# Kernel optimization log

Hardware: AMD Instinct MI355X
Metric: run time of the kernel (lower is better)

## Reference

```python
import jax, jax.numpy as jnp
import numpy as np

# ---- static config (mirrors GptOssDecoderLayer init) ----
H = 1024      # hidden_size
HD = 64       # head_size
NQ = 16       # num_query_heads
NKV = 4       # num_key_value_heads
G = NQ // NKV # num_key_value_groups
E = 8         # num_experts
TOPK = 2      # experts_per_token
FFN = 1024    # expert intermediate (== hidden in GPT-OSS)
B, Q = 4, 128 # batch sequences, new query tokens per sequence
P, PS = 8, 128
S = P * PS    # kv length per sequence
T = B * Q     # total query tokens
SW = 128      # sliding window (layer_idx % 2 == 0 -> active)
LIMIT = 7.0   # swiglu_limit
ALPHA = 1.702
EPS = 1e-5
NEG = -1e30
SCALE = HD ** -0.5


def rmsnorm(x, w):
    return x * w * jax.lax.rsqrt(jnp.mean(x * x, axis=-1, keepdims=True) + EPS)


def setup_inputs() -> dict:
    key = jax.random.key(0)
    ks = jax.random.split(key, 16)
    hidden = jax.random.normal(ks[0], (T, H), jnp.float32)
    kv_cache = jax.random.normal(ks[1], (B * P, 2, PS, NKV, HD), jnp.float32)
    kv_page_indices = jnp.arange(B * P, dtype=jnp.int32).reshape(B, P)
    # additive causal mask: query q sits at absolute position S - Q + q
    qpos = S - Q + jnp.arange(Q)
    kpos = jnp.arange(S)
    causal = qpos[:, None] >= kpos[None, :]
    attention_mask = jnp.broadcast_to(
        jnp.where(causal, 0.0, NEG).astype(jnp.float32), (B, Q, S))
    sinks = 0.1 * jax.random.normal(ks[2], (NQ,), jnp.float32)
    w_qkv = jax.random.normal(ks[3], (H, HD * (NQ + 2 * NKV)), jnp.float32) / np.sqrt(H)
    b_qkv = jnp.zeros((HD * (NQ + 2 * NKV),), jnp.float32)
    w_o = jax.random.normal(ks[4], (NQ * HD, H), jnp.float32) / np.sqrt(NQ * HD)
    b_o = jnp.zeros((H,), jnp.float32)
    ln1_w = jnp.ones((H,), jnp.float32)
    ln2_w = jnp.ones((H,), jnp.float32)
    w_router = jax.random.normal(ks[5], (H, E), jnp.float32) / np.sqrt(H)
    b_router = jnp.zeros((E,), jnp.float32)
    w_gate_up = jax.random.normal(ks[6], (E, H, 2 * FFN), jnp.float32) / np.sqrt(H)
    b_gate_up = jnp.zeros((E, 2 * FFN), jnp.float32)
    w_down = jax.random.normal(ks[7], (E, FFN, H), jnp.float32) / np.sqrt(FFN)
    b_down = jnp.zeros((E, H), jnp.float32)
    return dict(hidden=hidden, kv_cache=kv_cache, attention_mask=attention_mask,
                kv_page_indices=kv_page_indices, sinks=sinks, w_qkv=w_qkv,
                b_qkv=b_qkv, w_o=w_o, b_o=b_o, ln1_w=ln1_w, ln2_w=ln2_w,
                w_router=w_router, b_router=b_router, w_gate_up=w_gate_up,
                b_gate_up=b_gate_up, w_down=w_down, b_down=b_down)


def reference(hidden, kv_cache, attention_mask, kv_page_indices, sinks,
              w_qkv, b_qkv, w_o, b_o, ln1_w, ln2_w, w_router, b_router,
              w_gate_up, b_gate_up, w_down, b_down):
    # ---- attention block ----
    x = rmsnorm(hidden, ln1_w)
    qkv = x @ w_qkv + b_qkv                       # [T, HD*(NQ+2*NKV)]
    q = qkv[:, :NQ * HD].reshape(B, Q, NQ, HD)
    k_new = qkv[:, NQ * HD:(NQ + NKV) * HD].reshape(B, Q, NKV, HD)
    v_new = qkv[:, (NQ + NKV) * HD:].reshape(B, Q, NKV, HD)
    # gather paged KV cache -> [B, S, NKV, HD]; write new tokens into tail slots
    pages = kv_cache[kv_page_indices]             # [B, P, 2, PS, NKV, HD]
    K = pages[:, :, 0].reshape(B, S, NKV, HD).at[:, S - Q:].set(k_new)
    V = pages[:, :, 1].reshape(B, S, NKV, HD).at[:, S - Q:].set(v_new)
    Kr = jnp.repeat(K, G, axis=2)                 # GQA expand -> [B, S, NQ, HD]
    Vr = jnp.repeat(V, G, axis=2)
    scores = jnp.einsum('bqhd,bshd->bhqs', q * SCALE, Kr) + attention_mask[:, None]
    # sliding-window (module trims pages outside the window; equivalent mask)
    qpos = S - Q + jnp.arange(Q)
    kpos = jnp.arange(S)
    win_ok = (qpos[:, None] - kpos[None, :]) < SW
    scores = jnp.where(win_ok[None, None], scores, NEG)
    m = jnp.max(scores, axis=-1)
    m = jnp.where(jnp.isinf(m) & (m < 0), 0.0, m)
    p = jnp.exp(scores - m[..., None])            # [B, NQ, Q, S]
    # attention sink joins the softmax denominator (online-softmax correction)
    denom = jnp.sum(p, axis=-1) + jnp.exp(sinks[None, :, None] - m)
    attn = jnp.einsum('bhqs,bshd->bhqd', p, Vr) / denom[..., None]
    attn = attn.transpose(0, 2, 1, 3).reshape(T, NQ * HD)
    h = hidden + attn @ w_o + b_o
    # ---- MoE block ----
    x2 = rmsnorm(h, ln2_w)
    logits = x2 @ w_router + b_router             # [T, E]
    vals, idx = jax.lax.top_k(logits, TOPK)
    wts = jax.nn.softmax(vals, axis=-1)
    comb = jnp.sum(jax.nn.one_hot(idx, E, dtype=x2.dtype) * wts[..., None], axis=1)
    gu = jnp.einsum('th,ehf->etf', x2, w_gate_up) + b_gate_up[:, None, :]
    gate = jnp.minimum(gu[..., 0::2], LIMIT)
    up = jnp.clip(gu[..., 1::2], -LIMIT, LIMIT)
    glu = gate * jax.nn.sigmoid(gate * ALPHA)
    eo = jnp.einsum('etf,efh->eth', (up + 1.0) * glu, w_down) + b_down[:, None, :]
    moe = jnp.einsum('te,eth->th', comb, eo)
    return h + moe
```

## Files before the change

kernel.cpp:

```cpp
#include <hip/hip_runtime.h>

constexpr int H    = 1024;
constexpr int HD   = 64;
constexpr int NQ   = 16;
constexpr int NKV  = 4;
constexpr int E_   = 8;
constexpr int FFN  = 1024;
constexpr int B_   = 4;
constexpr int Q_   = 128;
constexpr int P_   = 8;
constexpr int PS   = 128;
constexpr int S_   = P_ * PS;
constexpr int T_   = B_ * Q_;
constexpr int QKV_N = HD * (NQ + 2 * NKV);
constexpr float EPS   = 1e-5f;
constexpr float ALPHA = 1.702f;
constexpr float LIMIT = 7.0f;
constexpr float SCALE = 0.125f;

constexpr int MAXROWS = 1536;

typedef __attribute__((ext_vector_type(4))) float f32x4;
typedef __attribute__((ext_vector_type(8))) short s16x8;

__device__ __forceinline__ unsigned short f2bf(float f) {
    unsigned u = __float_as_uint(f);
    u += 0x7FFFu + ((u >> 16) & 1u);
    return (unsigned short)(u >> 16);
}

__global__ __launch_bounds__(256) void repack_b_kernel(const float* __restrict__ src0,
                                                       unsigned short* __restrict__ dst0,
                                                       int N, size_t srcE, size_t dstE) {
    int e = blockIdx.z;
    const float* src = src0 + (size_t)e * srcE;
    unsigned short* dst = dst0 + (size_t)e * dstE;
    int nb = blockIdx.y;
    int kb = blockIdx.x * 4 + (threadIdx.x >> 6);
    int lane = threadIdx.x & 63;
    int kq = lane >> 4, c16 = lane & 15;
    const float* s = src + (size_t)(kb * 32 + kq * 8) * N + nb * 16 + c16;
    s16x8 p;
#pragma unroll
    for (int j = 0; j < 8; j++) p[j] = (short)f2bf(s[(size_t)j * N]);
    *(s16x8*)(dst + (((size_t)nb * 32 + kb) * 64 + lane) * 8) = p;
}

__global__ __launch_bounds__(256) void repack_gu_kernel(const float* __restrict__ wgu,
                                                        unsigned short* __restrict__ g,
                                                        unsigned short* __restrict__ u) {
    int e = blockIdx.z;
    int nb = blockIdx.y;
    int kb = blockIdx.x * 4 + (threadIdx.x >> 6);
    int lane = threadIdx.x & 63;
    int kq = lane >> 4, c16 = lane & 15;
    const float* s = wgu + ((size_t)e * 1024 + kb * 32 + kq * 8) * 2048 + 2 * (nb * 16 + c16);
    s16x8 pg, pu;
#pragma unroll
    for (int j = 0; j < 8; j++) {
        float2 v = *(const float2*)(s + (size_t)j * 2048);
        pg[j] = (short)f2bf(v.x);
        pu[j] = (short)f2bf(v.y);
    }
    size_t off = ((((size_t)e * 64 + nb) * 32 + kb) * 64 + lane) * 8;
    *(s16x8*)(g + off) = pg;
    *(s16x8*)(u + off) = pu;
}

__global__ __launch_bounds__(256) void rmsnorm_kernel(const float* __restrict__ in,
                                                      const float* __restrict__ w,
                                                      float* __restrict__ outf,
                                                      unsigned short* __restrict__ outb) {
    int t   = blockIdx.x;
    int tid = threadIdx.x;
    const float4* in4 = (const float4*)(in + (size_t)t * H);
    float4 v = in4[tid];
    float ss = v.x * v.x + v.y * v.y + v.z * v.z + v.w * v.w;
#pragma unroll
    for (int off = 32; off; off >>= 1) ss += __shfl_down(ss, off);
    __shared__ float partial[4];
    __shared__ float s_inv;
    if ((tid & 63) == 0) partial[tid >> 6] = ss;
    __syncthreads();
    if (tid == 0)
        s_inv = rsqrtf((partial[0] + partial[1] + partial[2] + partial[3]) * (1.0f / H) + EPS);
    __syncthreads();
    float inv = s_inv;
    float4 wv = ((const float4*)w)[tid];
    float4 o;
    o.x = v.x * wv.x * inv; o.y = v.y * wv.y * inv;
    o.z = v.z * wv.z * inv; o.w = v.w * wv.w * inv;
    if (outf) ((float4*)(outf + (size_t)t * H))[tid] = o;
    if (outb) {
        ushort4 ob;
        ob.x = f2bf(o.x); ob.y = f2bf(o.y); ob.z = f2bf(o.z); ob.w = f2bf(o.w);
        ((ushort4*)(outb + (size_t)t * H))[tid] = ob;
    }
}

__global__ __launch_bounds__(256) void gemm_splitk_bf16(const unsigned short* __restrict__ Abf,
                                                        const unsigned short* __restrict__ Bp,
                                                        const float* __restrict__ bias,
                                                        const float* __restrict__ resid,
                                                        float* __restrict__ C, int N) {
    int tid = threadIdx.x;
    int wv = tid >> 6, lane = tid & 63;
    int nb16 = blockIdx.x, mb = blockIdx.y * 64;
    int r16 = lane & 15, kq = lane >> 4;
    const unsigned short* ap = Abf + (size_t)(mb + r16) * 1024 + wv * 256 + kq * 8;
    const unsigned short* bp = Bp + (((size_t)nb16 * 32 + wv * 8) * 64 + lane) * 8;
    f32x4 acc[4] = {};
#pragma unroll 4
    for (int s = 0; s < 8; s++) {
        s16x8 af[4];
#pragma unroll
        for (int mt = 0; mt < 4; mt++)
            af[mt] = *(const s16x8*)(ap + mt * 16 * 1024 + s * 32);
        s16x8 bf = *(const s16x8*)(bp + s * 512);
#pragma unroll
        for (int mt = 0; mt < 4; mt++)
            acc[mt] = __builtin_amdgcn_mfma_f32_16x16x32_bf16(af[mt], bf, acc[mt], 0, 0, 0);
    }
    __shared__ float red[4][4][4][64];
#pragma unroll
    for (int mt = 0; mt < 4; mt++)
#pragma unroll
        for (int r = 0; r < 4; r++) red[wv][mt][r][lane] = acc[mt][r];
    __syncthreads();
    int mt = tid >> 6, li = tid & 63;
    int kq2 = li >> 4, c16 = li & 15;
    int col = nb16 * 16 + c16;
    float bcol = bias[col];
#pragma unroll
    for (int r = 0; r < 4; r++) {
        float s = red[0][mt][r][li] + red[1][mt][r][li] + red[2][mt][r][li] + red[3][mt][r][li];
        int row = mb + mt * 16 + kq2 * 4 + r;
        float v = s + bcol;
        if (resid) v += resid[(size_t)row * N + col];
        C[(size_t)row * N + col] = v;
    }
}

__global__ __launch_bounds__(256) void attn_group_kernel(const float* __restrict__ qkv,
                                                         const float* __restrict__ kv_cache,
                                                         const int* __restrict__ page_idx,
                                                         const float* __restrict__ sinks,
                                                         unsigned short* __restrict__ attn_bf) {
    int blk = blockIdx.x;
    int kvh = blk & 3;
    int q   = (blk >> 2) & 127;
    int b   = blk >> 9;
    int t   = b * Q_ + q;
    int tid = threadIdx.x;
    int s_lo = S_ - Q_ - 127 + q;

    __shared__ __align__(16) float Vs[128][64];
    __shared__ __align__(16) float qs4[4][64];
    __shared__ float pv[4][128];
    __shared__ float sD[4];

#pragma unroll
    for (int r = 0; r < 8; r++) {
        int l = r * 256 + tid;
        int key = l >> 4, c = l & 15;
        int s = s_lo + key;
        const float* vp;
        if (s < S_ - Q_) {
            int page = page_idx[b * P_ + (s >> 7)];
            vp = kv_cache + (size_t)page * 65536 + 32768 + (size_t)(s & 127) * (NKV * HD) + kvh * HD;
        } else {
            vp = qkv + (size_t)(b * Q_ + (s - (S_ - Q_))) * QKV_N + (NQ + NKV) * HD + kvh * HD;
        }
        ((float4*)Vs[key])[c] = *(const float4*)(vp + c * 4);
    }
    {
        int hh = tid >> 6, d = tid & 63;
        qs4[hh][d] = qkv[(size_t)t * QKV_N + (kvh * 4 + hh) * HD + d];
    }
    __syncthreads();

    {
        int key = tid & 127, hp = tid >> 7;
        int s = s_lo + key;
        const float* kp;
        if (s < S_ - Q_) {
            int page = page_idx[b * P_ + (s >> 7)];
            kp = kv_cache + (size_t)page * 65536 + (size_t)(s & 127) * (NKV * HD) + kvh * HD;
        } else {
            kp = qkv + (size_t)(b * Q_ + (s - (S_ - Q_))) * QKV_N + NQ * HD + kvh * HD;
        }
        const float4* kp4 = (const float4*)kp;
        const float4* q0p = (const float4*)qs4[hp * 2];
        const float4* q1p = (const float4*)qs4[hp * 2 + 1];
        float sc0 = 0.f, sc1 = 0.f;
#pragma unroll
        for (int d4 = 0; d4 < 16; d4++) {
            float4 kk = kp4[d4];
            float4 q0 = q0p[d4], q1 = q1p[d4];
            sc0 += q0.x * kk.x + q0.y * kk.y + q0.z * kk.z + q0.w * kk.w;
            sc1 += q1.x * kk.x + q1.y * kk.y + q1.z * kk.z + q1.w * kk.w;
        }
        pv[hp * 2][key]     = sc0 * SCALE;
        pv[hp * 2 + 1][key] = sc1 * SCALE;
    }
    __syncthreads();

    {
        int wv = tid >> 6, lane = tid & 63;
        float a0 = pv[wv][lane], a1 = pv[wv][lane + 64];
        float m = fmaxf(a0, a1);
#pragma unroll
        for (int off = 32; off; off >>= 1) m = fmaxf(m, __shfl_xor(m, off));
        float p0 = __expf(a0 - m), p1 = __expf(a1 - m);
        float l = p0 + p1;
#pragma unroll
        for (int off = 32; off; off >>= 1) l += __shfl_xor(l, off);
        pv[wv][lane] = p0;
        pv[wv][lane + 64] = p1;
        if (lane == 0) sD[wv] = l + __expf(sinks[kvh * 4 + wv] - m);
    }
    __syncthreads();

    {
        int hh = tid >> 6, d = tid & 63;
        float a0 = 0.f, a1 = 0.f, a2 = 0.f, a3 = 0.f;
#pragma unroll 4
        for (int i = 0; i < 128; i += 4) {
            a0 += pv[hh][i]     * Vs[i][d];
            a1 += pv[hh][i + 1] * Vs[i + 1][d];
            a2 += pv[hh][i + 2] * Vs[i + 2][d];
            a3 += pv[hh][i + 3] * Vs[i + 3][d];
        }
        float acc = ((a0 + a1) + (a2 + a3)) / sD[hh];
        attn_bf[(size_t)t * (NQ * HD) + (kvh * 4 + hh) * HD + d] = f2bf(acc);
    }
}

__global__ __launch_bounds__(64) void moe_zero_kernel(int* __restrict__ cnt, int* __restrict__ pos) {
    if (threadIdx.x < E_) { cnt[threadIdx.x] = 0; pos[threadIdx.x] = 0; }
}

__global__ __launch_bounds__(256) void router_kernel(const float* __restrict__ x2,
                                                     const float* __restrict__ w_router,
                                                     const float* __restrict__ b_router,
                                                     int* __restrict__ ridx,
                                                     float* __restrict__ rwt,
                                                     int* __restrict__ cnt) {
    int t = blockIdx.x;
    int tid = threadIdx.x;
    int e = tid >> 5;
    int j = tid & 31;
    float acc = 0.f;
    for (int hh = j; hh < H; hh += 32) acc += x2[(size_t)t * H + hh] * w_router[hh * E_ + e];
#pragma unroll
    for (int off = 16; off; off >>= 1) acc += __shfl_down(acc, off);
    __shared__ float logits[E_];
    if (j == 0) logits[e] = acc + b_router[e];
    __syncthreads();
    if (tid == 0) {
        int i0 = 0; float v0 = logits[0];
        for (int ee = 1; ee < E_; ee++)
            if (logits[ee] > v0) { v0 = logits[ee]; i0 = ee; }
        int i1 = -1; float v1 = -3.4e38f;
        for (int ee = 0; ee < E_; ee++)
            if (ee != i0 && logits[ee] > v1) { v1 = logits[ee]; i1 = ee; }
        float w0 = 1.0f / (1.0f + __expf(v1 - v0));
        ridx[t * 2] = i0; ridx[t * 2 + 1] = i1;
        rwt[t * 2] = w0;  rwt[t * 2 + 1] = 1.0f - w0;
        atomicAdd(&cnt[i0], 1);
        atomicAdd(&cnt[i1], 1);
    }
}

__global__ __launch_bounds__(64) void moe_offsets_kernel(const int* __restrict__ cnt,
                                                         int* __restrict__ poff) {
    if (threadIdx.x == 0) {
        int run = 0;
        for (int e = 0; e < E_; e++) { poff[e] = run; run += (cnt[e] + 63) & ~63; }
    }
}

__global__ __launch_bounds__(256) void moe_scatter_kernel(const int* __restrict__ ridx,
                                                          int* __restrict__ pos,
                                                          const int* __restrict__ poff,
                                                          int* __restrict__ list) {
    int i = blockIdx.x * 256 + threadIdx.x;
    if (i < 2 * T_) {
        int e = ridx[i];
        int p = atomicAdd(&pos[e], 1);
        list[poff[e] + p] = i;
    }
}

__global__ __launch_bounds__(256) void moe_gateup_sk(const unsigned short* __restrict__ x2bf,
                                                     const int* __restrict__ list,
                                                     const int* __restrict__ cnt,
                                                     const int* __restrict__ poff,
                                                     const unsigned short* __restrict__ wg,
                                                     const unsigned short* __restrict__ wu,
                                                     const float* __restrict__ b_gate_up,
                                                     unsigned short* __restrict__ act_bf) {
    int e  = blockIdx.y >> 4;
    int tl = blockIdx.y & 15;
    int n  = cnt[e];
    if (tl * 64 >= n) return;
    int base = poff[e];
    int nb = blockIdx.x;

    int tid = threadIdx.x;
    int wv = tid >> 6, lane = tid & 63;
    int r16 = lane & 15, kq = lane >> 4;
    const unsigned short* ap[4];
#pragma unroll
    for (int mt = 0; mt < 4; mt++) {
        int row = tl * 64 + mt * 16 + r16;
        int t2 = (row < n) ? list[base + row] : 0;
        ap[mt] = x2bf + (size_t)(t2 >> 1) * 1024 + wv * 256 + kq * 8;
    }
    size_t boff = ((((size_t)e * 64 + nb) * 32 + wv * 8) * 64 + lane) * 8;
    const unsigned short* gp = wg + boff;
    const unsigned short* up = wu + boff;

    f32x4 accg[4] = {}, accu[4] = {};
#pragma unroll 2
    for (int s = 0; s < 8; s++) {
        s16x8 af[4];
#pragma unroll
        for (int mt = 0; mt < 4; mt++) af[mt] = *(const s16x8*)(ap[mt] + s * 32);
        s16x8 bg = *(const s16x8*)(gp + s * 512);
        s16x8 bu = *(const s16x8*)(up + s * 512);
#pragma unroll
        for (int mt = 0; mt < 4; mt++) {
            accg[mt] = __builtin_amdgcn_mfma_f32_16x16x32_bf16(af[mt], bg, accg[mt], 0, 0, 0);
            accu[mt] = __builtin_amdgcn_mfma_f32_16x16x32_bf16(af[mt], bu, accu[mt], 0, 0, 0);
        }
    }
    __shared__ float redg[4][4][4][64];
    __shared__ float redu[4][4][4][64];
#pragma unroll
    for (int mt = 0; mt < 4; mt++)
#pragma unroll
        for (int r = 0; r < 4; r++) {
            redg[wv][mt][r][lane] = accg[mt][r];
            redu[wv][mt][r][lane] = accu[mt][r];
        }
    __syncthreads();
    int mt = tid >> 6, li = tid & 63;
    int kq2 = li >> 4, c16 = li & 15;
    int col = nb * 16 + c16;
    float bg_b = b_gate_up[(size_t)e * 2048 + 2 * col];
    float bu_b = b_gate_up[(size_t)e * 2048 + 2 * col + 1];
#pragma unroll
    for (int r = 0; r < 4; r++) {
        int rr = tl * 64 + mt * 16 + kq2 * 4 + r;
        if (rr < n) {
            float g = redg[0][mt][r][li] + redg[1][mt][r][li] + redg[2][mt][r][li] + redg[3][mt][r][li];
            float u = redu[0][mt][r][li] + redu[1][mt][r][li] + redu[2][mt][r][li] + redu[3][mt][r][li];
            float gate = fminf(g + bg_b, LIMIT);
            float up2 = fminf(fmaxf(u + bu_b, -LIMIT), LIMIT);
            float glu = gate / (1.0f + __expf(-ALPHA * gate));
            act_bf[(size_t)(base + rr) * FFN + col] = f2bf((up2 + 1.0f) * glu);
        }
    }
}

__global__ __launch_bounds__(256) void moe_down_sk(const unsigned short* __restrict__ act_bf,
                                                   const int* __restrict__ list,
                                                   const int* __restrict__ cnt,
                                                   const int* __restrict__ poff,
                                                   const float* __restrict__ rwt,
                                                   const unsigned short* __restrict__ wd,
                                                   const float* __restrict__ b_down,
                                                   float* __restrict__ part) {
    int e  = blockIdx.y >> 4;
    int tl = blockIdx.y & 15;
    int n  = cnt[e];
    if (tl * 64 >= n) return;
    int base = poff[e];
    int nb = blockIdx.x;

    int tid = threadIdx.x;
    int wv = tid >> 6, lane = tid & 63;
    int r16 = lane & 15, kq = lane >> 4;
    const unsigned short* ap = act_bf + (size_t)(base + tl * 64 + r16) * 1024 + wv * 256 + kq * 8;
    const unsigned short* bp = wd + ((size_t)e * 64 * 32 * 64 * 8) + (((size_t)nb * 32 + wv * 8) * 64 + lane) * 8;

    f32x4 acc[4] = {};
#pragma unroll 4
    for (int s = 0; s < 8; s++) {
        s16x8 af[4];
#pragma unroll
        for (int mt = 0; mt < 4; mt++) af[mt] = *(const s16x8*)(ap + mt * 16 * 1024 + s * 32);
        s16x8 bf = *(const s16x8*)(bp + s * 512);
#pragma unroll
        for (int mt = 0; mt < 4; mt++)
            acc[mt] = __builtin_amdgcn_mfma_f32_16x16x32_bf16(af[mt], bf, acc[mt], 0, 0, 0);
    }
    __shared__ float red[4][4][4][64];
#pragma unroll
    for (int mt = 0; mt < 4; mt++)
#pragma unroll
        for (int r = 0; r < 4; r++) red[wv][mt][r][lane] = acc[mt][r];
    __syncthreads();
    int mt = tid >> 6, li = tid & 63;
    int kq2 = li >> 4, c16 = li & 15;
    int col = nb * 16 + c16;
    float bcol = b_down[(size_t)e * 1024 + col];
#pragma unroll
    for (int r = 0; r < 4; r++) {
        int rr = tl * 64 + mt * 16 + kq2 * 4 + r;
        if (rr < n) {
            float s = red[0][mt][r][li] + red[1][mt][r][li] + red[2][mt][r][li] + red[3][mt][r][li];
            int t2 = list[base + rr];
            part[(size_t)t2 * H + col] = rwt[t2] * (s + bcol);
        }
    }
}

__global__ __launch_bounds__(256) void final_add_kernel(const float* __restrict__ hbuf,
                                                        const float* __restrict__ part,
                                                        float* __restrict__ out) {
    int t = blockIdx.x;
    int tid = threadIdx.x;
    float4 a  = ((const float4*)(hbuf + (size_t)t * H))[tid];
    float4 p0 = ((const float4*)(part + (size_t)(t * 2) * H))[tid];
    float4 p1 = ((const float4*)(part + (size_t)(t * 2 + 1) * H))[tid];
    float4 o;
    o.x = a.x + p0.x + p1.x; o.y = a.y + p0.y + p1.y;
    o.z = a.z + p0.z + p1.z; o.w = a.w + p0.w + p1.w;
    ((float4*)(out + (size_t)t * H))[tid] = o;
}

extern "C" void kernel_launch(void* const* d_in, const int* in_sizes, int n_in,
                              void* d_out, int out_size, void* d_ws, size_t ws_size,
                              hipStream_t stream) {
    const float* hidden          = (const float*)d_in[0];
    const float* kv_cache        = (const float*)d_in[1];
    const int*   kv_page_indices = (const int*)d_in[3];
    const float* sinks           = (const float*)d_in[4];
    const float* w_qkv           = (const float*)d_in[5];
    const float* b_qkv           = (const float*)d_in[6];
    const float* w_o             = (const float*)d_in[7];
    const float* b_o             = (const float*)d_in[8];
    const float* ln1_w           = (const float*)d_in[9];
    const float* ln2_w           = (const float*)d_in[10];
    const float* w_router        = (const float*)d_in[11];
    const float* b_router        = (const float*)d_in[12];
    const float* w_gate_up       = (const float*)d_in[13];
    const float* b_gate_up       = (const float*)d_in[14];
    const float* w_down          = (const float*)d_in[15];
    const float* b_down          = (const float*)d_in[16];
    float* out = (float*)d_out;

    char* base = (char*)d_ws;
    float* qkv   = (float*)base;                       base += (size_t)T_ * QKV_N * 4;
    float* hbuf  = (float*)base;                       base += (size_t)T_ * H * 4;
    float* x2    = (float*)base;                       base += (size_t)T_ * H * 4;
    float* part  = (float*)base;                       base += (size_t)2 * T_ * H * 4;
    unsigned short* x_bf    = (unsigned short*)base;   base += (size_t)T_ * H * 2;
    unsigned short* x2_bf   = (unsigned short*)base;   base += (size_t)T_ * H * 2;
    unsigned short* attn_bf = (unsigned short*)base;   base += (size_t)T_ * NQ * HD * 2;
    unsigned short* act_bf  = (unsigned short*)base;   base += (size_t)MAXROWS * FFN * 2;
    unsigned short* wq_bf   = (unsigned short*)base;   base += (size_t)H * QKV_N * 2;
    unsigned short* wo_bf   = (unsigned short*)base;   base += (size_t)H * H * 2;
    unsigned short* wg_bf   = (unsigned short*)base;   base += (size_t)E_ * H * FFN * 2;
    unsigned short* wu_bf   = (unsigned short*)base;   base += (size_t)E_ * H * FFN * 2;
    unsigned short* wd_bf   = (unsigned short*)base;   base += (size_t)E_ * FFN * H * 2;
    float* rwt = (float*)base;                         base += 2 * T_ * 4;
    int*   ridx = (int*)base;                          base += 2 * T_ * 4;
    int*   cnt  = (int*)base;                          base += E_ * 4;
    int*   pos  = (int*)base;                          base += E_ * 4;
    int*   poff = (int*)base;                          base += E_ * 4;
    int*   list = (int*)base;                          base += MAXROWS * 4;

    moe_zero_kernel<<<1, 64, 0, stream>>>(cnt, pos);
    repack_gu_kernel<<<dim3(8, 64, 8), 256, 0, stream>>>(w_gate_up, wg_bf, wu_bf);
    repack_b_kernel<<<dim3(8, 64, 8), 256, 0, stream>>>(w_down, wd_bf, H,
                                                        (size_t)FFN * H, (size_t)64 * 32 * 64 * 8);
    repack_b_kernel<<<dim3(8, QKV_N / 16, 1), 256, 0, stream>>>(w_qkv, wq_bf, QKV_N, 0, 0);
    repack_b_kernel<<<dim3(8, H / 16, 1), 256, 0, stream>>>(w_o, wo_bf, H, 0, 0);

    rmsnorm_kernel<<<T_, 256, 0, stream>>>(hidden, ln1_w, nullptr, x_bf);
    gemm_splitk_bf16<<<dim3(QKV_N / 16, T_ / 64), 256, 0, stream>>>(x_bf, wq_bf, b_qkv, nullptr, qkv, QKV_N);
    attn_group_kernel<<<B_ * Q_ * NKV, 256, 0, stream>>>(qkv, kv_cache, kv_page_indices, sinks, attn_bf);
    gemm_splitk_bf16<<<dim3(H / 16, T_ / 64), 256, 0, stream>>>(attn_bf, wo_bf, b_o, hidden, hbuf, H);
    rmsnorm_kernel<<<T_, 256, 0, stream>>>(hbuf, ln2_w, x2, x2_bf);
    router_kernel<<<T_, 256, 0, stream>>>(x2, w_router, b_router, ridx, rwt, cnt);
    moe_offsets_kernel<<<1, 64, 0, stream>>>(cnt, poff);
    moe_scatter_kernel<<<(2 * T_ + 255) / 256, 256, 0, stream>>>(ridx, pos, poff, list);
    moe_gateup_sk<<<dim3(FFN / 16, E_ * 16), 256, 0, stream>>>(
        x2_bf, list, cnt, poff, wg_bf, wu_bf, b_gate_up, act_bf);
    moe_down_sk<<<dim3(H / 16, E_ * 16), 256, 0, stream>>>(
        act_bf, list, cnt, poff, rwt, wd_bf, b_down, part);
    final_add_kernel<<<T_, 256, 0, stream>>>(hbuf, part, out);
}
```

Before: 329.8 us.

## Fuse repacks, rmsnorm+router, MoE plumbing; atomic-add MoE output; 128-row expert tiles

Merges the four weight-repack launches and the counter zeroing into one kernel. Fuses the second RMSNorm with the router and merges offset computation with scatter into a single-block kernel. The down projection now atomically adds weighted results straight into the output, which the O-projection GEMM pre-seeds with the residual, so the partial buffer and final add kernel go away. Expert GEMM tiles grow from 64 to 128 rows to reuse each B fragment across more MFMAs, at the cost of more registers and float-atomic nondeterminism.

```diff
diff --git a/kernel.cpp b/kernel.cpp
--- a/kernel.cpp
+++ b/kernel.cpp
@@ -29,52 +29,70 @@
     return (unsigned short)(u >> 16);
 }
 
-__global__ __launch_bounds__(256) void repack_b_kernel(const float* __restrict__ src0,
-                                                       unsigned short* __restrict__ dst0,
-                                                       int N, size_t srcE, size_t dstE) {
-    int e = blockIdx.z;
-    const float* src = src0 + (size_t)e * srcE;
-    unsigned short* dst = dst0 + (size_t)e * dstE;
-    int nb = blockIdx.y;
-    int kb = blockIdx.x * 4 + (threadIdx.x >> 6);
-    int lane = threadIdx.x & 63;
+__global__ __launch_bounds__(256) void repack_all_kernel(const float* __restrict__ wgu,
+                                                         const float* __restrict__ wdn,
+                                                         const float* __restrict__ wqkv,
+                                                         const float* __restrict__ wo,
+                                                         unsigned short* __restrict__ g,
+                                                         unsigned short* __restrict__ u,
+                                                         unsigned short* __restrict__ d,
+                                                         unsigned short* __restrict__ q,
+                                                         unsigned short* __restrict__ o,
+                                                         int* __restrict__ cnt) {
+    int idx = blockIdx.x;
+    int tid = threadIdx.x;
+    if (idx == 0 && tid < E_) cnt[tid] = 0;
+    int lane = tid & 63;
     int kq = lane >> 4, c16 = lane & 15;
-    const float* s = src + (size_t)(kb * 32 + kq * 8) * N + nb * 16 + c16;
-    s16x8 p;
-#pragma unroll
-    for (int j = 0; j < 8; j++) p[j] = (short)f2bf(s[(size_t)j * N]);
-    *(s16x8*)(dst + (((size_t)nb * 32 + kb) * 64 + lane) * 8) = p;
-}
-
-__global__ __launch_bounds__(256) void repack_gu_kernel(const float* __restrict__ wgu,
-                                                        unsigned short* __restrict__ g,
-                                                        unsigned short* __restrict__ u) {
-    int e = blockIdx.z;
-    int nb = blockIdx.y;
-    int kb = blockIdx.x * 4 + (threadIdx.x >> 6);
-    int lane = threadIdx.x & 63;
-    int kq = lane >> 4, c16 = lane & 15;
-    const float* s = wgu + ((size_t)e * 1024 + kb * 32 + kq * 8) * 2048 + 2 * (nb * 16 + c16);
-    s16x8 pg, pu;
-#pragma unroll
-    for (int j = 0; j < 8; j++) {
-        float2 v = *(const float2*)(s + (size_t)j * 2048);
-        pg[j] = (short)f2bf(v.x);
-        pu[j] = (short)f2bf(v.y);
-    }
-    size_t off = ((((size_t)e * 64 + nb) * 32 + kb) * 64 + lane) * 8;
-    *(s16x8*)(g + off) = pg;
-    *(s16x8*)(u + off) = pu;
+    if (idx < 4096) {
+        int e = idx >> 9, rem = idx & 511;
+        int nb = rem >> 3, kb = (rem & 7) * 4 + (tid >> 6);
+        const float* s = wgu + ((size_t)e * 1024 + kb * 32 + kq * 8) * 2048 + 2 * (nb * 16 + c16);
+        s16x8 pg, pu;
+#pragma unroll
+        for (int j = 0; j < 8; j++) {
+            float2 v = *(const float2*)(s + (size_t)j * 2048);
+            pg[j] = (short)f2bf(v.x);
+            pu[j] = (short)f2bf(v.y);
+        }
+        size_t off = ((((size_t)e * 64 + nb) * 32 + kb) * 64 + lane) * 8;
+        *(s16x8*)(g + off) = pg;
+        *(s16x8*)(u + off) = pu;
+    } else if (idx < 8192) {
+        int i2 = idx - 4096;
+        int e = i2 >> 9, rem = i2 & 511;
+        int nb = rem >> 3, kb = (rem & 7) * 4 + (tid >> 6);
+        const float* s = wdn + (size_t)e * FFN * H + (size_t)(kb * 32 + kq * 8) * 1024 + nb * 16 + c16;
+        s16x8 p;
+#pragma unroll
+        for (int j = 0; j < 8; j++) p[j] = (short)f2bf(s[(size_t)j * 1024]);
+        size_t off = (size_t)e * (64 * 32 * 64 * 8) + (((size_t)nb * 32 + kb) * 64 + lane) * 8;
+        *(s16x8*)(d + off) = p;
+    } else if (idx < 8960) {
+        int i2 = idx - 8192;
+        int nb = i2 >> 3, kb = (i2 & 7) * 4 + (tid >> 6);
+        const float* s = wqkv + (size_t)(kb * 32 + kq * 8) * QKV_N + nb * 16 + c16;
+        s16x8 p;
+#pragma unroll
+        for (int j = 0; j < 8; j++) p[j] = (short)f2bf(s[(size_t)j * QKV_N]);
+        *(s16x8*)(q + (((size_t)nb * 32 + kb) * 64 + lane) * 8) = p;
+    } else {
+        int i2 = idx - 8960;
+        int nb = i2 >> 3, kb = (i2 & 7) * 4 + (tid >> 6);
+        const float* s = wo + (size_t)(kb * 32 + kq * 8) * H + nb * 16 + c16;
+        s16x8 p;
+#pragma unroll
+        for (int j = 0; j < 8; j++) p[j] = (short)f2bf(s[(size_t)j * H]);
+        *(s16x8*)(o + (((size_t)nb * 32 + kb) * 64 + lane) * 8) = p;
+    }
 }
 
 __global__ __launch_bounds__(256) void rmsnorm_kernel(const float* __restrict__ in,
                                                       const float* __restrict__ w,
-                                                      float* __restrict__ outf,
                                                       unsigned short* __restrict__ outb) {
     int t   = blockIdx.x;
     int tid = threadIdx.x;
-    const float4* in4 = (const float4*)(in + (size_t)t * H);
-    float4 v = in4[tid];
+    float4 v = ((const float4*)(in + (size_t)t * H))[tid];
     float ss = v.x * v.x + v.y * v.y + v.z * v.z + v.w * v.w;
 #pragma unroll
     for (int off = 32; off; off >>= 1) ss += __shfl_down(ss, off);
@@ -87,22 +105,18 @@
     __syncthreads();
     float inv = s_inv;
     float4 wv = ((const float4*)w)[tid];
-    float4 o;
-    o.x = v.x * wv.x * inv; o.y = v.y * wv.y * inv;
-    o.z = v.z * wv.z * inv; o.w = v.w * wv.w * inv;
-    if (outf) ((float4*)(outf + (size_t)t * H))[tid] = o;
-    if (outb) {
-        ushort4 ob;
-        ob.x = f2bf(o.x); ob.y = f2bf(o.y); ob.z = f2bf(o.z); ob.w = f2bf(o.w);
-        ((ushort4*)(outb + (size_t)t * H))[tid] = ob;
-    }
+    ushort4 ob;
+    ob.x = f2bf(v.x * wv.x * inv); ob.y = f2bf(v.y * wv.y * inv);
+    ob.z = f2bf(v.z * wv.z * inv); ob.w = f2bf(v.w * wv.w * inv);
+    ((ushort4*)(outb + (size_t)t * H))[tid] = ob;
 }
 
 __global__ __launch_bounds__(256) void gemm_splitk_bf16(const unsigned short* __restrict__ Abf,
                                                         const unsigned short* __restrict__ Bp,
                                                         const float* __restrict__ bias,
                                                         const float* __restrict__ resid,
-                                                        float* __restrict__ C, int N) {
+                                                        float* __restrict__ C,
+                                                        float* __restrict__ Cdup, int N) {
     int tid = threadIdx.x;
     int wv = tid >> 6, lane = tid & 63;
     int nb16 = blockIdx.x, mb = blockIdx.y * 64;
@@ -138,6 +152,7 @@
         float v = s + bcol;
         if (resid) v += resid[(size_t)row * N + col];
         C[(size_t)row * N + col] = v;
+        if (Cdup) Cdup[(size_t)row * N + col] = v;
     }
 }
 
@@ -174,8 +189,8 @@
         ((float4*)Vs[key])[c] = *(const float4*)(vp + c * 4);
     }
     {
-        int hh = tid >> 6, d = tid & 63;
-        qs4[hh][d] = qkv[(size_t)t * QKV_N + (kvh * 4 + hh) * HD + d];
+        int hh = tid >> 6, d2 = tid & 63;
+        qs4[hh][d2] = qkv[(size_t)t * QKV_N + (kvh * 4 + hh) * HD + d2];
     }
     __syncthreads();
 
@@ -222,40 +237,79 @@
     __syncthreads();
 
     {
-        int hh = tid >> 6, d = tid & 63;
+        int hh = tid >> 6, d2 = tid & 63;
         float a0 = 0.f, a1 = 0.f, a2 = 0.f, a3 = 0.f;
 #pragma unroll 4
         for (int i = 0; i < 128; i += 4) {
-            a0 += pv[hh][i]     * Vs[i][d];
-            a1 += pv[hh][i + 1] * Vs[i + 1][d];
-            a2 += pv[hh][i + 2] * Vs[i + 2][d];
-            a3 += pv[hh][i + 3] * Vs[i + 3][d];
+            a0 += pv[hh][i]     * Vs[i][d2];
+            a1 += pv[hh][i + 1] * Vs[i + 1][d2];
+            a2 += pv[hh][i + 2] * Vs[i + 2][d2];
+            a3 += pv[hh][i + 3] * Vs[i + 3][d2];
         }
         float acc = ((a0 + a1) + (a2 + a3)) / sD[hh];
-        attn_bf[(size_t)t * (NQ * HD) + (kvh * 4 + hh) * HD + d] = f2bf(acc);
-    }
-}
-
-__global__ __launch_bounds__(64) void moe_zero_kernel(int* __restrict__ cnt, int* __restrict__ pos) {
-    if (threadIdx.x < E_) { cnt[threadIdx.x] = 0; pos[threadIdx.x] = 0; }
-}
-
-__global__ __launch_bounds__(256) void router_kernel(const float* __restrict__ x2,
-                                                     const float* __restrict__ w_router,
-                                                     const float* __restrict__ b_router,
-                                                     int* __restrict__ ridx,
-                                                     float* __restrict__ rwt,
-                                                     int* __restrict__ cnt) {
+        attn_bf[(size_t)t * (NQ * HD) + (kvh * 4 + hh) * HD + d2] = f2bf(acc);
+    }
+}
+
+__global__ __launch_bounds__(256) void rms_router_kernel(const float* __restrict__ hbuf,
+                                                         const float* __restrict__ ln2w,
+                                                         const float* __restrict__ w_router,
+                                                         const float* __restrict__ b_router,
+                                                         unsigned short* __restrict__ x2bf,
+                                                         int* __restrict__ ridx,
+                                                         float* __restrict__ rwt,
+                                                         int* __restrict__ cnt) {
     int t = blockIdx.x;
     int tid = threadIdx.x;
-    int e = tid >> 5;
-    int j = tid & 31;
-    float acc = 0.f;
-    for (int hh = j; hh < H; hh += 32) acc += x2[(size_t)t * H + hh] * w_router[hh * E_ + e];
-#pragma unroll
-    for (int off = 16; off; off >>= 1) acc += __shfl_down(acc, off);
+    float4 v = ((const float4*)(hbuf + (size_t)t * H))[tid];
+    float ss = v.x * v.x + v.y * v.y + v.z * v.z + v.w * v.w;
+#pragma unroll
+    for (int off = 32; off; off >>= 1) ss += __shfl_down(ss, off);
+    __shared__ float partial[4];
+    __shared__ float s_inv;
+    if ((tid & 63) == 0) partial[tid >> 6] = ss;
+    __syncthreads();
+    if (tid == 0)
+        s_inv = rsqrtf((partial[0] + partial[1] + partial[2] + partial[3]) * (1.0f / H) + EPS);
+    __syncthreads();
+    float inv = s_inv;
+    float4 wv = ((const float4*)ln2w)[tid];
+    float4 o;
+    o.x = v.x * wv.x * inv; o.y = v.y * wv.y * inv;
+    o.z = v.z * wv.z * inv; o.w = v.w * wv.w * inv;
+    ushort4 ob;
+    ob.x = f2bf(o.x); ob.y = f2bf(o.y); ob.z = f2bf(o.z); ob.w = f2bf(o.w);
+    ((ushort4*)(x2bf + (size_t)t * H))[tid] = ob;
+
+    const float4* wr = (const float4*)(w_router + (size_t)tid * 4 * E_);
+    float p[E_];
+    {
+        float4 r0a = wr[0], r0b = wr[1];
+        float4 r1a = wr[2], r1b = wr[3];
+        float4 r2a = wr[4], r2b = wr[5];
+        float4 r3a = wr[6], r3b = wr[7];
+        p[0] = o.x * r0a.x + o.y * r1a.x + o.z * r2a.x + o.w * r3a.x;
+        p[1] = o.x * r0a.y + o.y * r1a.y + o.z * r2a.y + o.w * r3a.y;
+        p[2] = o.x * r0a.z + o.y * r1a.z + o.z * r2a.z + o.w * r3a.z;
+        p[3] = o.x * r0a.w + o.y * r1a.w + o.z * r2a.w + o.w * r3a.w;
+        p[4] = o.x * r0b.x + o.y * r1b.x + o.z * r2b.x + o.w * r3b.x;
+        p[5] = o.x * r0b.y + o.y * r1b.y + o.z * r2b.y + o.w * r3b.y;
+        p[6] = o.x * r0b.z + o.y * r1b.z + o.z * r2b.z + o.w * r3b.z;
+        p[7] = o.x * r0b.w + o.y * r1b.w + o.z * r2b.w + o.w * r3b.w;
+    }
+    __shared__ float wsum[4][E_];
+    int wv2 = tid >> 6, lane = tid & 63;
+#pragma unroll
+    for (int e = 0; e < E_; e++) {
+        float r = p[e];
+#pragma unroll
+        for (int off = 32; off; off >>= 1) r += __shfl_xor(r, off);
+        if (lane == 0) wsum[wv2][e] = r;
+    }
+    __syncthreads();
     __shared__ float logits[E_];
-    if (j == 0) logits[e] = acc + b_router[e];
+    if (tid < E_)
+        logits[tid] = wsum[0][tid] + wsum[1][tid] + wsum[2][tid] + wsum[3][tid] + b_router[tid];
     __syncthreads();
     if (tid == 0) {
         int i0 = 0; float v0 = logits[0];
@@ -272,23 +326,22 @@
     }
 }
 
-__global__ __launch_bounds__(64) void moe_offsets_kernel(const int* __restrict__ cnt,
-                                                         int* __restrict__ poff) {
-    if (threadIdx.x == 0) {
+__global__ __launch_bounds__(256) void plumb_kernel(const int* __restrict__ cnt,
+                                                    const int* __restrict__ ridx,
+                                                    int* __restrict__ poff,
+                                                    int* __restrict__ list) {
+    __shared__ int lpos[E_], lpoff[E_];
+    int tid = threadIdx.x;
+    if (tid == 0) {
         int run = 0;
-        for (int e = 0; e < E_; e++) { poff[e] = run; run += (cnt[e] + 63) & ~63; }
-    }
-}
-
-__global__ __launch_bounds__(256) void moe_scatter_kernel(const int* __restrict__ ridx,
-                                                          int* __restrict__ pos,
-                                                          const int* __restrict__ poff,
-                                                          int* __restrict__ list) {
-    int i = blockIdx.x * 256 + threadIdx.x;
-    if (i < 2 * T_) {
+        for (int e = 0; e < E_; e++) { lpoff[e] = run; poff[e] = run; run += (cnt[e] + 63) & ~63; }
+    }
+    if (tid < E_) lpos[tid] = 0;
+    __syncthreads();
+    for (int i = tid; i < 2 * T_; i += 256) {
         int e = ridx[i];
-        int p = atomicAdd(&pos[e], 1);
-        list[poff[e] + p] = i;
+        int pp = atomicAdd(&lpos[e], 1);
+        list[lpoff[e] + pp] = i;
     }
 }
 
@@ -300,20 +353,20 @@
                                                      const unsigned short* __restrict__ wu,
                                                      const float* __restrict__ b_gate_up,
                                                      unsigned short* __restrict__ act_bf) {
-    int e  = blockIdx.y >> 4;
-    int tl = blockIdx.y & 15;
+    int e  = blockIdx.y >> 3;
+    int tl = blockIdx.y & 7;
     int n  = cnt[e];
-    if (tl * 64 >= n) return;
+    if (tl * 128 >= n) return;
     int base = poff[e];
     int nb = blockIdx.x;
 
     int tid = threadIdx.x;
     int wv = tid >> 6, lane = tid & 63;
     int r16 = lane & 15, kq = lane >> 4;
-    const unsigned short* ap[4];
-#pragma unroll
-    for (int mt = 0; mt < 4; mt++) {
-        int row = tl * 64 + mt * 16 + r16;
+    const unsigned short* ap[8];
+#pragma unroll
+    for (int mt = 0; mt < 8; mt++) {
+        int row = tl * 128 + mt * 16 + r16;
         int t2 = (row < n) ? list[base + row] : 0;
         ap[mt] = x2bf + (size_t)(t2 >> 1) * 1024 + wv * 256 + kq * 8;
     }
@@ -321,45 +374,47 @@
     const unsigned short* gp = wg + boff;
     const unsigned short* up = wu + boff;
 
-    f32x4 accg[4] = {}, accu[4] = {};
+    f32x4 accg[8] = {}, accu[8] = {};
 #pragma unroll 2
     for (int s = 0; s < 8; s++) {
-        s16x8 af[4];
-#pragma unroll
-        for (int mt = 0; mt < 4; mt++) af[mt] = *(const s16x8*)(ap[mt] + s * 32);
         s16x8 bg = *(const s16x8*)(gp + s * 512);
         s16x8 bu = *(const s16x8*)(up + s * 512);
 #pragma unroll
-        for (int mt = 0; mt < 4; mt++) {
-            accg[mt] = __builtin_amdgcn_mfma_f32_16x16x32_bf16(af[mt], bg, accg[mt], 0, 0, 0);
-            accu[mt] = __builtin_amdgcn_mfma_f32_16x16x32_bf16(af[mt], bu, accu[mt], 0, 0, 0);
+        for (int mt = 0; mt < 8; mt++) {
+            s16x8 af = *(const s16x8*)(ap[mt] + s * 32);
+            accg[mt] = __builtin_amdgcn_mfma_f32_16x16x32_bf16(af, bg, accg[mt], 0, 0, 0);
+            accu[mt] = __builtin_amdgcn_mfma_f32_16x16x32_bf16(af, bu, accu[mt], 0, 0, 0);
         }
     }
     __shared__ float redg[4][4][4][64];
     __shared__ float redu[4][4][4][64];
-#pragma unroll
-    for (int mt = 0; mt < 4; mt++)
-#pragma unroll
-        for (int r = 0; r < 4; r++) {
-            redg[wv][mt][r][lane] = accg[mt][r];
-            redu[wv][mt][r][lane] = accu[mt][r];
-        }
-    __syncthreads();
-    int mt = tid >> 6, li = tid & 63;
-    int kq2 = li >> 4, c16 = li & 15;
-    int col = nb * 16 + c16;
+    int col = nb * 16 + (tid & 15);
     float bg_b = b_gate_up[(size_t)e * 2048 + 2 * col];
     float bu_b = b_gate_up[(size_t)e * 2048 + 2 * col + 1];
 #pragma unroll
-    for (int r = 0; r < 4; r++) {
-        int rr = tl * 64 + mt * 16 + kq2 * 4 + r;
-        if (rr < n) {
-            float g = redg[0][mt][r][li] + redg[1][mt][r][li] + redg[2][mt][r][li] + redg[3][mt][r][li];
-            float u = redu[0][mt][r][li] + redu[1][mt][r][li] + redu[2][mt][r][li] + redu[3][mt][r][li];
-            float gate = fminf(g + bg_b, LIMIT);
-            float up2 = fminf(fmaxf(u + bu_b, -LIMIT), LIMIT);
-            float glu = gate / (1.0f + __expf(-ALPHA * gate));
-            act_bf[(size_t)(base + rr) * FFN + col] = f2bf((up2 + 1.0f) * glu);
+    for (int h = 0; h < 2; h++) {
+        __syncthreads();
+#pragma unroll
+        for (int m2 = 0; m2 < 4; m2++)
+#pragma unroll
+            for (int r = 0; r < 4; r++) {
+                redg[wv][m2][r][lane] = accg[h * 4 + m2][r];
+                redu[wv][m2][r][lane] = accu[h * 4 + m2][r];
+            }
+        __syncthreads();
+        int m2 = tid >> 6, li = tid & 63;
+        int kq2 = li >> 4;
+#pragma unroll
+        for (int r = 0; r < 4; r++) {
+            int rr = tl * 128 + (h * 4 + m2) * 16 + kq2 * 4 + r;
+            if (rr < n) {
+                float g = redg[0][m2][r][li] + redg[1][m2][r][li] + redg[2][m2][r][li] + redg[3][m2][r][li];
+                float u = redu[0][m2][r][li] + redu[1][m2][r][li] + redu[2][m2][r][li] + redu[3][m2][r][li];
+                float gate = fminf(g + bg_b, LIMIT);
+                float up2 = fminf(fmaxf(u + bu_b, -LIMIT), LIMIT);
+                float glu = gate / (1.0f + __expf(-ALPHA * gate));
+                act_bf[(size_t)(base + rr) * FFN + col] = f2bf((up2 + 1.0f) * glu);
+            }
         }
     }
 }
@@ -371,64 +426,53 @@
                                                    const float* __restrict__ rwt,
                                                    const unsigned short* __restrict__ wd,
                                                    const float* __restrict__ b_down,
-                                                   float* __restrict__ part) {
-    int e  = blockIdx.y >> 4;
-    int tl = blockIdx.y & 15;
+                                                   float* __restrict__ out) {
+    int e  = blockIdx.y >> 3;
+    int tl = blockIdx.y & 7;
     int n  = cnt[e];
-    if (tl * 64 >= n) return;
+    if (tl * 128 >= n) return;
     int base = poff[e];
     int nb = blockIdx.x;
 
     int tid = threadIdx.x;
     int wv = tid >> 6, lane = tid & 63;
     int r16 = lane & 15, kq = lane >> 4;
-    const unsigned short* ap = act_bf + (size_t)(base + tl * 64 + r16) * 1024 + wv * 256 + kq * 8;
-    const unsigned short* bp = wd + ((size_t)e * 64 * 32 * 64 * 8) + (((size_t)nb * 32 + wv * 8) * 64 + lane) * 8;
-
-    f32x4 acc[4] = {};
-#pragma unroll 4
+    const unsigned short* ap = act_bf + (size_t)(base + tl * 128 + r16) * 1024 + wv * 256 + kq * 8;
+    const unsigned short* bp = wd + (size_t)e * (64 * 32 * 64 * 8) + (((size_t)nb * 32 + wv * 8) * 64 + lane) * 8;
+
+    f32x4 acc[8] = {};
+#pragma unroll 2
     for (int s = 0; s < 8; s++) {
-        s16x8 af[4];
-#pragma unroll
-        for (int mt = 0; mt < 4; mt++) af[mt] = *(const s16x8*)(ap + mt * 16 * 1024 + s * 32);
         s16x8 bf = *(const s16x8*)(bp + s * 512);
 #pragma unroll
-        for (int mt = 0; mt < 4; mt++)
-            acc[mt] = __builtin_amdgcn_mfma_f32_16x16x32_bf16(af[mt], bf, acc[mt], 0, 0, 0);
+        for (int mt = 0; mt < 8; mt++) {
+            s16x8 af = *(const s16x8*)(ap + mt * 16 * 1024 + s * 32);
+            acc[mt] = __builtin_amdgcn_mfma_f32_16x16x32_bf16(af, bf, acc[mt], 0, 0, 0);
+        }
     }
     __shared__ float red[4][4][4][64];
-#pragma unroll
-    for (int mt = 0; mt < 4; mt++)
-#pragma unroll
-        for (int r = 0; r < 4; r++) red[wv][mt][r][lane] = acc[mt][r];
-    __syncthreads();
-    int mt = tid >> 6, li = tid & 63;
-    int kq2 = li >> 4, c16 = li & 15;
-    int col = nb * 16 + c16;
+    int col = nb * 16 + (tid & 15);
     float bcol = b_down[(size_t)e * 1024 + col];
 #pragma unroll
-    for (int r = 0; r < 4; r++) {
-        int rr = tl * 64 + mt * 16 + kq2 * 4 + r;
-        if (rr < n) {
-            float s = red[0][mt][r][li] + red[1][mt][r][li] + red[2][mt][r][li] + red[3][mt][r][li];
-            int t2 = list[base + rr];
-            part[(size_t)t2 * H + col] = rwt[t2] * (s + bcol);
-        }
-    }
-}
-
-__global__ __launch_bounds__(256) void final_add_kernel(const float* __restrict__ hbuf,
-                                                        const float* __restrict__ part,
-                                                        float* __restrict__ out) {
-    int t = blockIdx.x;
-    int tid = threadIdx.x;
-    float4 a  = ((const float4*)(hbuf + (size_t)t * H))[tid];
-    float4 p0 = ((const float4*)(part + (size_t)(t * 2) * H))[tid];
-    float4 p1 = ((const float4*)(part + (size_t)(t * 2 + 1) * H))[tid];
-    float4 o;
-    o.x = a.x + p0.x + p1.x; o.y = a.y + p0.y + p1.y;
-    o.z = a.z + p0.z + p1.z; o.w = a.w + p0.w + p1.w;
-    ((float4*)(out + (size_t)t * H))[tid] = o;
+    for (int h = 0; h < 2; h++) {
+        __syncthreads();
+#pragma unroll
+        for (int m2 = 0; m2 < 4; m2++)
+#pragma unroll
+            for (int r = 0; r < 4; r++) red[wv][m2][r][lane] = acc[h * 4 + m2][r];
+        __syncthreads();
+        int m2 = tid >> 6, li = tid & 63;
+        int kq2 = li >> 4;
+#pragma unroll
+        for (int r = 0; r < 4; r++) {
+            int rr = tl * 128 + (h * 4 + m2) * 16 + kq2 * 4 + r;
+            if (rr < n) {
+                float s = red[0][m2][r][li] + red[1][m2][r][li] + red[2][m2][r][li] + red[3][m2][r][li];
+                int t2 = list[base + rr];
+                atomicAdd(&out[(size_t)(t2 >> 1) * H + col], rwt[t2] * (s + bcol));
+            }
+        }
+    }
 }
 
 extern "C" void kernel_launch(void* const* d_in, const int* in_sizes, int n_in,
@@ -455,42 +499,34 @@
     char* base = (char*)d_ws;
     float* qkv   = (float*)base;                       base += (size_t)T_ * QKV_N * 4;
     float* hbuf  = (float*)base;                       base += (size_t)T_ * H * 4;
-    float* x2    = (float*)base;                       base += (size_t)T_ * H * 4;
-    float* part  = (float*)base;                       base += (size_t)2 * T_ * H * 4;
     unsigned short* x_bf    = (unsigned short*)base;   base += (size_t)T_ * H * 2;
     unsigned short* x2_bf   = (unsigned short*)base;   base += (size_t)T_ * H * 2;
     unsigned short* attn_bf = (unsigned short*)base;   base += (size_t)T_ * NQ * HD * 2;
-    unsigned short* act_bf  = (unsigned short*)base;   base += (size_t)MAXROWS * FFN * 2;
+    unsigned short* act_bf  = (unsigned short*)base;   base += (size_t)(MAXROWS + 128) * FFN * 2;
     unsigned short* wq_bf   = (unsigned short*)base;   base += (size_t)H * QKV_N * 2;
     unsigned short* wo_bf   = (unsigned short*)base;   base += (size_t)H * H * 2;
     unsigned short* wg_bf   = (unsigned short*)base;   base += (size_t)E_ * H * FFN * 2;
     unsigned short* wu_bf   = (unsigned short*)base;   base += (size_t)E_ * H * FFN * 2;
     unsigned short* wd_bf   = (unsigned short*)base;   base += (size_t)E_ * FFN * H * 2;
-    float* rwt = (float*)base;                         base += 2 * T_ * 4;
+    float* rwt  = (float*)base;                        base += 2 * T_ * 4;
     int*   ridx = (int*)base;                          base += 2 * T_ * 4;
     int*   cnt  = (int*)base;                          base += E_ * 4;
-    int*   pos  = (int*)base;                          base += E_ * 4;
     int*   poff = (int*)base;                          base += E_ * 4;
     int*   list = (int*)base;                          base += MAXROWS * 4;
 
-    moe_zero_kernel<<<1, 64, 0, stream>>>(cnt, pos);
-    repack_gu_kernel<<<dim3(8, 64, 8), 256, 0, stream>>>(w_gate_up, wg_bf, wu_bf);
-    repack_b_kernel<<<dim3(8, 64, 8), 256, 0, stream>>>(w_down, wd_bf, H,
-                                                        (size_t)FFN * H, (size_t)64 * 32 * 64 * 8);
-    repack_b_kernel<<<dim3(8, QKV_N / 16, 1), 256, 0, stream>>>(w_qkv, wq_bf, QKV_N, 0, 0);
-    repack_b_kernel<<<dim3(8, H / 16, 1), 256, 0, stream>>>(w_o, wo_bf, H, 0, 0);
-
-    rmsnorm_kernel<<<T_, 256, 0, stream>>>(hidden, ln1_w, nullptr, x_bf);
-    gemm_splitk_bf16<<<dim3(QKV_N / 16, T_ / 64), 256, 0, stream>>>(x_bf, wq_bf, b_qkv, nullptr, qkv, QKV_N);
+    repack_all_kernel<<<9472, 256, 0, stream>>>(w_gate_up, w_down, w_qkv, w_o,
+                                                wg_bf, wu_bf, wd_bf, wq_bf, wo_bf, cnt);
+    rmsnorm_kernel<<<T_, 256, 0, stream>>>(hidden, ln1_w, x_bf);
+    gemm_splitk_bf16<<<dim3(QKV_N / 16, T_ / 64), 256, 0, stream>>>(
+        x_bf, wq_bf, b_qkv, nullptr, qkv, nullptr, QKV_N);
     attn_group_kernel<<<B_ * Q_ * NKV, 256, 0, stream>>>(qkv, kv_cache, kv_page_indices, sinks, attn_bf);
-    gemm_splitk_bf16<<<dim3(H / 16, T_ / 64), 256, 0, stream>>>(attn_bf, wo_bf, b_o, hidden, hbuf, H);
-    rmsnorm_kernel<<<T_, 256, 0, stream>>>(hbuf, ln2_w, x2, x2_bf);
-    router_kernel<<<T_, 256, 0, stream>>>(x2, w_router, b_router, ridx, rwt, cnt);
-    moe_offsets_kernel<<<1, 64, 0, stream>>>(cnt, poff);
-    moe_scatter_kernel<<<(2 * T_ + 255) / 256, 256, 0, stream>>>(ridx, pos, poff, list);
-    moe_gateup_sk<<<dim3(FFN / 16, E_ * 16), 256, 0, stream>>>(
+    gemm_splitk_bf16<<<dim3(H / 16, T_ / 64), 256, 0, stream>>>(
+        attn_bf, wo_bf, b_o, hidden, hbuf, out, H);
+    rms_router_kernel<<<T_, 256, 0, stream>>>(hbuf, ln2_w, w_router, b_router,
+                                              x2_bf, ridx, rwt, cnt);
+    plumb_kernel<<<1, 256, 0, stream>>>(cnt, ridx, poff, list);
+    moe_gateup_sk<<<dim3(FFN / 16, E_ * 8), 256, 0, stream>>>(
         x2_bf, list, cnt, poff, wg_bf, wu_bf, b_gate_up, act_bf);
-    moe_down_sk<<<dim3(H / 16, E_ * 16), 256, 0, stream>>>(
-        act_bf, list, cnt, poff, rwt, wd_bf, b_down, part);
-    final_add_kernel<<<T_, 256, 0, stream>>>(hbuf, part, out);
-}
+    moe_down_sk<<<dim3(H / 16, E_ * 8), 256, 0, stream>>>(
+        act_bf, list, cnt, poff, rwt, wd_bf, b_down, out);
+}
```

After: 310.1 us. 6.0% less time.
